# Performance work log

Hardware: AMD Instinct MI355X
Metric: run time of the kernel (lower is better)

The kernel has to match this reference:

```python
import jax, jax.numpy as jnp
import numpy as np

ALPHA = 0.5
BETA = 5.0
LOGIT_SCALE = 100.0  # exp(log(100)) -- CLIP's learned logit scale at its clamp value
NUM_CLASSES = 200


def _l2norm(x):
    return x / jnp.linalg.norm(x, axis=-1, keepdims=True)


def setup_inputs() -> dict:
    key = jax.random.key(0)
    k1, k2, k3, k4 = jax.random.split(key, 4)
    img_f = jax.random.normal(k1, (1024, 512), dtype=jnp.float32)
    text_features = jax.random.normal(k2, (200, 512), dtype=jnp.float32)
    keys = jax.random.normal(k3, (50000, 512), dtype=jnp.float32)
    labels = jax.random.randint(k4, (50000,), 0, NUM_CLASSES, dtype=jnp.int64)
    return {"img_f": img_f, "text_features": text_features, "keys": keys, "labels": labels}


def reference(img_f, text_features, keys, labels):
    # encode_image output is L2-normalized in the module; keys were built from
    # normalized image features, text_features are normalized class embeddings.
    q = _l2norm(img_f)            # [B, D]
    t = _l2norm(text_features)    # [C, D]
    k = _l2norm(keys)             # [N, D]

    # CLIP zero-shot branch: scale * q @ t.T -> [B, C]
    z = LOGIT_SCALE * jnp.einsum('bd,cd->bc', q, t)

    # Tip-Adapter cache branch: exp(beta * q @ keys.T) @ one_hot(labels)
    sim = jnp.einsum('bd,nd->bn', q, k)                 # [B, N]
    aff = jnp.exp(BETA * sim)                           # [B, N]
    values = jax.nn.one_hot(labels, NUM_CLASSES, dtype=aff.dtype)  # [N, C]
    c = aff @ values                                    # [B, C]

    return (1.0 - ALPHA) * z + ALPHA * c
```

## Files before the change

### kernel.cpp

```cpp
#include <hip/hip_runtime.h>

#define B_Q    1024
#define D_K    512
#define N_CLS  200
#define N_KEYS 50000
#define N_PAD  50048
#define N_ZT   (N_PAD / 128)
#define NT_TOT (N_ZT + 2)
#define KN_ROWS 50304

#define R0 N_PAD
#define R1 (R0 + B_Q)
#define R2 (R1 + N_CLS)
#define R3 (R2 + 56)
#define R4 (R3 + 400)

typedef __attribute__((ext_vector_type(8))) short bf16x8;
typedef __attribute__((ext_vector_type(4))) float f32x4;

__device__ __forceinline__ unsigned short f2bf(float f) {
  union { float f; unsigned int i; } v; v.f = f;
  unsigned int r = v.i + 0x7fffu + ((v.i >> 16) & 1u);
  return (unsigned short)(r >> 16);
}
__device__ __forceinline__ uint4 pack8(const float f[8], float s) {
  uint4 o;
  o.x = (unsigned)f2bf(f[0]*s) | ((unsigned)f2bf(f[1]*s) << 16);
  o.y = (unsigned)f2bf(f[2]*s) | ((unsigned)f2bf(f[3]*s) << 16);
  o.z = (unsigned)f2bf(f[4]*s) | ((unsigned)f2bf(f[5]*s) << 16);
  o.w = (unsigned)f2bf(f[6]*s) | ((unsigned)f2bf(f[7]*s) << 16);
  return o;
}
__device__ __forceinline__ void async_copy16(const void* g, void* lds) {
  __builtin_amdgcn_global_load_lds(
      (const __attribute__((address_space(1))) unsigned int*)g,
      (__attribute__((address_space(3))) unsigned int*)lds, 16, 0, 0);
}

__global__ __launch_bounds__(1024) void k_rank(const int* __restrict__ labels,
                                               int* __restrict__ perm,
                                               int* __restrict__ cls) {
  __shared__ int hall[N_CLS];
  __shared__ int hbef[N_CLS];
  __shared__ int incl[N_CLS];
  __shared__ int lcur[N_CLS];
  int t = threadIdx.x;
  int base = blockIdx.x * 1024;
  if (t < N_CLS) { hall[t] = 0; hbef[t] = 0; lcur[t] = 0; }
  __syncthreads();
  for (int idx = t; idx < N_KEYS; idx += 1024) {
    int lab = labels[idx];
    atomicAdd(&hall[lab], 1);
    if (idx < base) atomicAdd(&hbef[lab], 1);
  }
  __syncthreads();
  if (t < N_CLS) incl[t] = hall[t];
  __syncthreads();
  for (int d = 1; d < N_CLS; d <<= 1) {
    int x = 0;
    if (t < N_CLS && t >= d) x = incl[t - d];
    __syncthreads();
    if (t < N_CLS) incl[t] += x;
    __syncthreads();
  }
  int n = base + t;
  if (n < N_KEYS) {
    int lab = labels[n];
    int r = atomicAdd(&lcur[lab], 1);
    int d = (incl[lab] - hall[lab]) + hbef[lab] + r;
    perm[d] = n;
    cls[d] = lab;
  } else if (n < KN_ROWS) {
    perm[n] = n;
    cls[n] = N_CLS;
  }
}

__global__ void k_prep2(const float* __restrict__ keys, const float* __restrict__ img,
                        const float* __restrict__ txt,
                        unsigned short* __restrict__ qn, unsigned short* __restrict__ kn,
                        float* __restrict__ out) {
  int w = threadIdx.x >> 6, lane = threadIdx.x & 63;
  int row = blockIdx.x * 4 + w;
  const float* src; unsigned short* dst;
  if (row < R0) {
    if (row >= N_KEYS) {
      *((uint4*)(kn + (size_t)row * D_K) + lane) = make_uint4(0, 0, 0, 0);
      return;
    }
    src = keys + (size_t)row * D_K;
    dst = kn + (size_t)row * D_K;
  } else if (row < R1) {
    int r = row - R0;
    src = img + (size_t)r * D_K;
    dst = qn + (size_t)r * D_K;
  } else if (row < R2) {
    int r = row - R1;
    src = txt + (size_t)r * D_K;
    dst = kn + (size_t)(N_PAD + r) * D_K;
  } else if (row < R3) {
    int r = N_PAD + N_CLS + (row - R2);
    *((uint4*)(kn + (size_t)r * D_K) + lane) = make_uint4(0, 0, 0, 0);
    return;
  } else if (row < R4) {
    int zr = row - R3;
    uint4* o4 = (uint4*)(out + (size_t)zr * 512) + lane * 2;
    o4[0] = make_uint4(0, 0, 0, 0);
    o4[1] = make_uint4(0, 0, 0, 0);
    return;
  } else return;
  const float4* s4 = (const float4*)src + lane * 2;
  float4 a = s4[0], b = s4[1];
  float f[8] = {a.x, a.y, a.z, a.w, b.x, b.y, b.z, b.w};
  float ss = 0.f;
#pragma unroll
  for (int i = 0; i < 8; i++) ss += f[i] * f[i];
#pragma unroll
  for (int d = 1; d < 64; d <<= 1) ss += __shfl_xor(ss, d);
  float rinv = rsqrtf(ss);
  *((uint4*)dst + lane) = pack8(f, rinv);
}

__global__ __launch_bounds__(256, 3) void k_main(const unsigned short* __restrict__ qn,
                                                 const unsigned short* __restrict__ kn,
                                                 const int* __restrict__ cls,
                                                 const int* __restrict__ perm,
                                                 float* __restrict__ out) {
  __shared__ unsigned short As[128 * 64];
  __shared__ unsigned short Bs[128 * 64];
  int t = threadIdx.x;
  int wsw = (blockIdx.x & 7) * NT_TOT + (blockIdx.x >> 3);
  int tileN = wsw >> 3, tileB = wsw & 7;
  int rowB0 = tileB * 128, rowN0 = tileN * 128;

  f32x4 acc[4][4];
#pragma unroll
  for (int i = 0; i < 4; i++)
#pragma unroll
    for (int j = 0; j < 4; j++) acc[i][j] = (f32x4){0.f, 0.f, 0.f, 0.f};

  int lane = t & 63, w = t >> 6;
  int wr = (w >> 1) * 64, wc = (w & 1) * 64;
  int l15 = lane & 15, lq = lane >> 4;
  const int rA = t >> 3;
  const int gsw = ((t & 7) ^ (rA & 7)) * 8;
  const int sw = l15 & 7;

  int prow[4];
#pragma unroll
  for (int i = 0; i < 4; i++) prow[i] = perm[rowN0 + i * 32 + rA];
  int cj[4];
#pragma unroll
  for (int j = 0; j < 4; j++) cj[j] = cls[rowN0 + wc + 16 * j + l15];
  int cseg0 = cls[rowN0 + wc];
  int cseg1 = cls[rowN0 + wc + 63];

  for (int k0 = 0; k0 < D_K; k0 += 64) {
    __syncthreads();
#pragma unroll
    for (int i = 0; i < 4; i++) {
      int row = i * 32 + rA;
      async_copy16(qn + (size_t)(rowB0 + row) * D_K + k0 + gsw, &As[i * 2048 + t * 8]);
      async_copy16(kn + (size_t)prow[i] * D_K + k0 + gsw, &Bs[i * 2048 + t * 8]);
    }
    __syncthreads();
#pragma unroll
    for (int ks = 0; ks < 64; ks += 32) {
      bf16x8 af[4], bf[4];
#pragma unroll
      for (int i = 0; i < 4; i++)
        af[i] = *(const bf16x8*)&As[(wr + 16 * i + l15) * 64 + ((((ks >> 3) + lq) ^ sw) * 8)];
#pragma unroll
      for (int j = 0; j < 4; j++)
        bf[j] = *(const bf16x8*)&Bs[(wc + 16 * j + l15) * 64 + ((((ks >> 3) + lq) ^ sw) * 8)];
#pragma unroll
      for (int i = 0; i < 4; i++)
#pragma unroll
        for (int j = 0; j < 4; j++)
          acc[i][j] = __builtin_amdgcn_mfma_f32_16x16x32_bf16(af[i], bf[j], acc[i][j], 0, 0, 0);
    }
  }

  if (tileN >= N_ZT) {
#pragma unroll
    for (int i = 0; i < 4; i++)
#pragma unroll
      for (int j = 0; j < 4; j++) {
        int col = rowN0 + wc + 16 * j + l15 - N_PAD;
        if (col < N_CLS) {
#pragma unroll
          for (int r = 0; r < 4; r++) {
            int row = rowB0 + wr + 16 * i + lq * 4 + r;
            atomicAdd(out + (size_t)row * N_CLS + col, 50.0f * acc[i][j][r]);
          }
        }
      }
    return;
  }

#pragma unroll
  for (int i = 0; i < 4; i++)
#pragma unroll
    for (int j = 0; j < 4; j++)
#pragma unroll
      for (int r = 0; r < 4; r++) acc[i][j][r] = __expf(5.0f * acc[i][j][r]);

  for (int c = cseg0; c <= cseg1; c++) {
    if (c >= N_CLS) break;
#pragma unroll
    for (int i = 0; i < 4; i++) {
      float s0 = 0.f, s1 = 0.f, s2 = 0.f, s3 = 0.f;
#pragma unroll
      for (int j = 0; j < 4; j++) {
        if (cj[j] == c) {
          s0 += acc[i][j][0]; s1 += acc[i][j][1];
          s2 += acc[i][j][2]; s3 += acc[i][j][3];
        }
      }
#pragma unroll
      for (int d = 1; d < 16; d <<= 1) {
        s0 += __shfl_xor(s0, d); s1 += __shfl_xor(s1, d);
        s2 += __shfl_xor(s2, d); s3 += __shfl_xor(s3, d);
      }
      if (l15 == 0) {
        int row = rowB0 + wr + 16 * i + lq * 4;
        float* o = out + (size_t)row * N_CLS + c;
        if (s0 != 0.f) atomicAdd(o + 0 * N_CLS, 0.5f * s0);
        if (s1 != 0.f) atomicAdd(o + 1 * N_CLS, 0.5f * s1);
        if (s2 != 0.f) atomicAdd(o + 2 * N_CLS, 0.5f * s2);
        if (s3 != 0.f) atomicAdd(o + 3 * N_CLS, 0.5f * s3);
      }
    }
  }
}

extern "C" void kernel_launch(void* const* d_in, const int* in_sizes, int n_in,
                              void* d_out, int out_size, void* d_ws, size_t ws_size,
                              hipStream_t stream) {
  (void)in_sizes; (void)n_in; (void)out_size; (void)ws_size;
  const float* img    = (const float*)d_in[0];
  const float* txt    = (const float*)d_in[1];
  const float* keys   = (const float*)d_in[2];
  const int*   labels = (const int*)d_in[3];
  float*       out    = (float*)d_out;

  char* ws = (char*)d_ws;
  unsigned short* qn = (unsigned short*)(ws + 0);
  unsigned short* kn = (unsigned short*)(ws + 1048576);
  int*  perm = (int*)(ws + 52559872);
  int*  cls  = (int*)(ws + 52761088);

  k_rank<<<(KN_ROWS + 1023) / 1024, 1024, 0, stream>>>(labels, perm, cls);
  k_prep2<<<(R4 + 3) / 4, 256, 0, stream>>>(keys, img, txt, qn, kn, out);
  k_main<<<dim3(8 * NT_TOT), 256, 0, stream>>>(qn, kn, cls, perm, out);
}
```

Baseline: 267.9 us.

## Double-buffer LDS tiles in main GEMM and merge rank/prep kernels

The main kernel now uses two 32-wide K LDS buffers, so the async global-to-LDS copy of the next slice overlaps the MFMA work on the current one. This replaces the old scheme of a load, a barrier and then compute, and it uses a new XOR swizzle for the narrower rows. Separately, the label-ranking kernel and the normalize/convert kernel are fused into a single launch. The ranking part now runs as 197 blocks of 256 threads, each rescanning all labels. The price is more barriers per K step and redundant histogram work across more blocks.

```diff
diff --git a/kernel.cpp b/kernel.cpp
--- a/kernel.cpp
+++ b/kernel.cpp
@@ -8,6 +8,7 @@
 #define N_ZT   (N_PAD / 128)
 #define NT_TOT (N_ZT + 2)
 #define KN_ROWS 50304
+#define RANK_BLKS 197
 
 #define R0 N_PAD
 #define R1 (R0 + B_Q)
@@ -37,51 +38,54 @@
       (__attribute__((address_space(3))) unsigned int*)lds, 16, 0, 0);
 }
 
-__global__ __launch_bounds__(1024) void k_rank(const int* __restrict__ labels,
-                                               int* __restrict__ perm,
-                                               int* __restrict__ cls) {
-  __shared__ int hall[N_CLS];
-  __shared__ int hbef[N_CLS];
-  __shared__ int incl[N_CLS];
-  __shared__ int lcur[N_CLS];
-  int t = threadIdx.x;
-  int base = blockIdx.x * 1024;
-  if (t < N_CLS) { hall[t] = 0; hbef[t] = 0; lcur[t] = 0; }
-  __syncthreads();
-  for (int idx = t; idx < N_KEYS; idx += 1024) {
-    int lab = labels[idx];
-    atomicAdd(&hall[lab], 1);
-    if (idx < base) atomicAdd(&hbef[lab], 1);
-  }
-  __syncthreads();
-  if (t < N_CLS) incl[t] = hall[t];
-  __syncthreads();
-  for (int d = 1; d < N_CLS; d <<= 1) {
-    int x = 0;
-    if (t < N_CLS && t >= d) x = incl[t - d];
-    __syncthreads();
-    if (t < N_CLS) incl[t] += x;
-    __syncthreads();
-  }
-  int n = base + t;
-  if (n < N_KEYS) {
-    int lab = labels[n];
-    int r = atomicAdd(&lcur[lab], 1);
-    int d = (incl[lab] - hall[lab]) + hbef[lab] + r;
-    perm[d] = n;
-    cls[d] = lab;
-  } else if (n < KN_ROWS) {
-    perm[n] = n;
-    cls[n] = N_CLS;
-  }
-}
-
-__global__ void k_prep2(const float* __restrict__ keys, const float* __restrict__ img,
-                        const float* __restrict__ txt,
-                        unsigned short* __restrict__ qn, unsigned short* __restrict__ kn,
-                        float* __restrict__ out) {
+__global__ __launch_bounds__(256) void k_aux(const float* __restrict__ keys,
+                                             const float* __restrict__ img,
+                                             const float* __restrict__ txt,
+                                             const int* __restrict__ labels,
+                                             unsigned short* __restrict__ qn,
+                                             unsigned short* __restrict__ kn,
+                                             int* __restrict__ perm,
+                                             int* __restrict__ cls,
+                                             float* __restrict__ out) {
+  if (blockIdx.x < RANK_BLKS) {
+    __shared__ int hall[N_CLS];
+    __shared__ int hbef[N_CLS];
+    __shared__ int incl[N_CLS];
+    __shared__ int lcur[N_CLS];
+    int t = threadIdx.x;
+    int base = blockIdx.x * 256;
+    if (t < N_CLS) { hall[t] = 0; hbef[t] = 0; lcur[t] = 0; }
+    __syncthreads();
+    for (int idx = t; idx < N_KEYS; idx += 256) {
+      int lab = labels[idx];
+      atomicAdd(&hall[lab], 1);
+      if (idx < base) atomicAdd(&hbef[lab], 1);
+    }
+    __syncthreads();
+    if (t < N_CLS) incl[t] = hall[t];
+    __syncthreads();
+    for (int d = 1; d < N_CLS; d <<= 1) {
+      int x = 0;
+      if (t < N_CLS && t >= d) x = incl[t - d];
+      __syncthreads();
+      if (t < N_CLS) incl[t] += x;
+      __syncthreads();
+    }
+    int n = base + t;
+    if (n < N_KEYS) {
+      int lab = labels[n];
+      int r = atomicAdd(&lcur[lab], 1);
+      int d = (incl[lab] - hall[lab]) + hbef[lab] + r;
+      perm[d] = n;
+      cls[d] = lab;
+    } else if (n < KN_ROWS) {
+      perm[n] = n;
+      cls[n] = N_CLS;
+    }
+    return;
+  }
   int w = threadIdx.x >> 6, lane = threadIdx.x & 63;
-  int row = blockIdx.x * 4 + w;
+  int row = (blockIdx.x - RANK_BLKS) * 4 + w;
   const float* src; unsigned short* dst;
   if (row < R0) {
     if (row >= N_KEYS) {
@@ -126,8 +130,8 @@
                                                  const int* __restrict__ cls,
                                                  const int* __restrict__ perm,
                                                  float* __restrict__ out) {
-  __shared__ unsigned short As[128 * 64];
-  __shared__ unsigned short Bs[128 * 64];
+  __shared__ unsigned short As[2][128 * 32];
+  __shared__ unsigned short Bs[2][128 * 32];
   int t = threadIdx.x;
   int wsw = (blockIdx.x & 7) * NT_TOT + (blockIdx.x >> 3);
   int tileN = wsw >> 3, tileB = wsw & 7;
@@ -142,44 +146,53 @@
   int lane = t & 63, w = t >> 6;
   int wr = (w >> 1) * 64, wc = (w & 1) * 64;
   int l15 = lane & 15, lq = lane >> 4;
-  const int rA = t >> 3;
-  const int gsw = ((t & 7) ^ (rA & 7)) * 8;
-  const int sw = l15 & 7;
-
-  int prow[4];
-#pragma unroll
-  for (int i = 0; i < 4; i++) prow[i] = perm[rowN0 + i * 32 + rA];
+  const int r0 = t >> 2;
+  const int fr = (r0 ^ (r0 >> 2)) & 3;
+  const int gsw = ((t & 3) ^ fr) * 8;
+
+  int prow0 = perm[rowN0 + r0];
+  int prow1 = perm[rowN0 + r0 + 64];
   int cj[4];
 #pragma unroll
   for (int j = 0; j < 4; j++) cj[j] = cls[rowN0 + wc + 16 * j + l15];
   int cseg0 = cls[rowN0 + wc];
   int cseg1 = cls[rowN0 + wc + 63];
 
-  for (int k0 = 0; k0 < D_K; k0 += 64) {
-    __syncthreads();
+  auto stage = [&](int p, int k0) {
+    async_copy16(qn + (size_t)(rowB0 + r0) * D_K + k0 + gsw,      &As[p][t * 8]);
+    async_copy16(qn + (size_t)(rowB0 + r0 + 64) * D_K + k0 + gsw, &As[p][2048 + t * 8]);
+    async_copy16(kn + (size_t)prow0 * D_K + k0 + gsw,             &Bs[p][t * 8]);
+    async_copy16(kn + (size_t)prow1 * D_K + k0 + gsw,             &Bs[p][2048 + t * 8]);
+  };
+  auto compute = [&](int p) {
+    bf16x8 af[4], bf[4];
 #pragma unroll
     for (int i = 0; i < 4; i++) {
-      int row = i * 32 + rA;
-      async_copy16(qn + (size_t)(rowB0 + row) * D_K + k0 + gsw, &As[i * 2048 + t * 8]);
-      async_copy16(kn + (size_t)prow[i] * D_K + k0 + gsw, &Bs[i * 2048 + t * 8]);
-    }
-    __syncthreads();
-#pragma unroll
-    for (int ks = 0; ks < 64; ks += 32) {
-      bf16x8 af[4], bf[4];
-#pragma unroll
-      for (int i = 0; i < 4; i++)
-        af[i] = *(const bf16x8*)&As[(wr + 16 * i + l15) * 64 + ((((ks >> 3) + lq) ^ sw) * 8)];
+      int ra = wr + 16 * i + l15;
+      af[i] = *(const bf16x8*)&As[p][ra * 32 + ((lq ^ ((ra ^ (ra >> 2)) & 3)) * 8)];
+    }
+#pragma unroll
+    for (int j = 0; j < 4; j++) {
+      int rb = wc + 16 * j + l15;
+      bf[j] = *(const bf16x8*)&Bs[p][rb * 32 + ((lq ^ ((rb ^ (rb >> 2)) & 3)) * 8)];
+    }
+#pragma unroll
+    for (int i = 0; i < 4; i++)
 #pragma unroll
       for (int j = 0; j < 4; j++)
-        bf[j] = *(const bf16x8*)&Bs[(wc + 16 * j + l15) * 64 + ((((ks >> 3) + lq) ^ sw) * 8)];
-#pragma unroll
-      for (int i = 0; i < 4; i++)
-#pragma unroll
-        for (int j = 0; j < 4; j++)
-          acc[i][j] = __builtin_amdgcn_mfma_f32_16x16x32_bf16(af[i], bf[j], acc[i][j], 0, 0, 0);
-    }
-  }
+        acc[i][j] = __builtin_amdgcn_mfma_f32_16x16x32_bf16(af[i], bf[j], acc[i][j], 0, 0, 0);
+  };
+
+  stage(0, 0);
+  __syncthreads();
+#pragma unroll
+  for (int k0 = 32; k0 < D_K; k0 += 32) {
+    int p = ((k0 >> 5) - 1) & 1;
+    stage(p ^ 1, k0);
+    compute(p);
+    __syncthreads();
+  }
+  compute(1);
 
   if (tileN >= N_ZT) {
 #pragma unroll
@@ -250,7 +263,7 @@
   int*  perm = (int*)(ws + 52559872);
   int*  cls  = (int*)(ws + 52761088);
 
-  k_rank<<<(KN_ROWS + 1023) / 1024, 1024, 0, stream>>>(labels, perm, cls);
-  k_prep2<<<(R4 + 3) / 4, 256, 0, stream>>>(keys, img, txt, qn, kn, out);
+  k_aux<<<RANK_BLKS + (R4 + 3) / 4, 256, 0, stream>>>(keys, img, txt, labels,
+                                                      qn, kn, perm, cls, out);
   k_main<<<dim3(8 * NT_TOT), 256, 0, stream>>>(qn, kn, cls, perm, out);
 }
```

Result: slower. 333.1 us (+24.3%).
